# Optimization experiments

Hardware: AMD Instinct MI355X
Metric: run time of the kernel (lower is better)

## Reference

```python
import jax, jax.numpy as jnp
import numpy as np

N = 20000; DX = 512; DW = 64; DY = 256; M = 320000
DS = DX // 2; DD = DX // 4; DP = DS + DD  # 256, 128, 384
EPS = 1e-9; LN_EPS = 1e-5; SLOPE = 0.05
PNAMES = ['rW1','rb1','rg1','rbt1','rW2','rb2','yW1','yb1','yg1','ybt1','yW2','yb2',
          'iaW1','iab1','iag1','iabt1','iaW2','iab2','cW1','cb1','cg1','cbt1','cW2','cb2']

def _mlp2(h, W1, b1, g, be, W2, b2):
    # Linear -> LayerNorm -> LeakyReLU(0.05) -> Linear  (matches mlp(..., norm='layer'))
    h = h @ W1 + b1
    mu = jnp.mean(h, axis=-1, keepdims=True)
    var = jnp.mean((h - mu) ** 2, axis=-1, keepdims=True)
    h = (h - mu) * jax.lax.rsqrt(var + LN_EPS) * g + be
    h = jnp.where(h >= 0, h, SLOPE * h)
    return h @ W2 + b2

def _m(Pp, n, h):
    return _mlp2(h, Pp[n+'W1'], Pp[n+'b1'], Pp[n+'g1'], Pp[n+'bt1'], Pp[n+'W2'], Pp[n+'b2'])

def _agg(a, b):
    s = a + b
    return jnp.where(s >= 0, s, SLOPE * s)

def _run(x, ei, edge_attr, u_r, u_ia, u_pick, Pp, dec=None):
    """GuoUnpool forward (steps 1a, 2a, 2b). ei: concrete numpy [2,M] int64.
    dec holds concrete sampled decisions; built from the uniforms when None."""
    build = dec is None
    if build:
        dec = {}
    # coalesce (edges are duplicate-free) + lexsort by (src, dst)
    perm = np.argsort(ei[0].astype(np.int64) * N + ei[1].astype(np.int64), kind='stable')
    src, dst = ei[0][perm], ei[1][perm]
    ea = edge_attr[perm]
    # --- step 1a: bernoulli unpool decision per node (I_s = I_u = empty, I_r = all nodes)
    pr = jax.nn.sigmoid(_m(Pp, 'r', x)[:, 0])
    if build:
        dec['choose'] = np.asarray(u_r) < np.asarray(pr)
    choose = dec['choose']
    Iu = np.flatnonzero(choose); Is = np.flatnonzero(~choose)
    logP = jnp.sum(jnp.where(jnp.asarray(choose), jnp.log(pr + EPS), jnp.log(1.0 - pr + EPS)))
    prs = jnp.clip(pr, EPS, 1.0 - EPS)
    ent = -jnp.sum(prs * jnp.log(prs) + (1.0 - prs) * jnp.log(1.0 - prs))
    # --- projections (_ps1_idx = [0:ds+D], _ps2_idx = [0:ds] + [ds+D:ds+2D]) and child embeddings
    ps1 = x[:, :DP]
    ps2 = jnp.concatenate([x[:, :DS], x[:, DS + DD:DS + 2 * DD]], axis=-1)
    y1 = _m(Pp, 'y', ps1)   # [N, dy]; rows at Is give x_static, rows at Iu give x_c1
    y2 = _m(Pp, 'y', ps2)   # rows at Iu give x_c2
    x_out = jnp.concatenate([y1[Is], y1[Iu], y2[Iu]], axis=0)
    # --- step 2a: intra-edge decision for unpooled nodes
    p_ia = jax.nn.sigmoid(_m(Pp, 'ia', _agg(y1[Iu], y2[Iu]))[:, 0])
    if build:
        dec['vc'] = np.asarray(u_ia)[Iu] < np.asarray(p_ia)
    vc = dec['vc']
    logP = logP + jnp.sum(jnp.where(jnp.asarray(vc), jnp.log(p_ia + EPS), jnp.log(1.0 - p_ia + EPS)))
    ps = jnp.clip(p_ia, EPS, 1.0 - EPS)
    ent = ent - jnp.sum(ps * jnp.log(ps) + (1.0 - ps) * jnp.log(1.0 - ps))
    # --- step 2b: categorical neighbor pick for unpooled nodes without intra edge
    if build:
        iun = Iu[~vc]
        par = np.concatenate([src, dst]); nb = np.concatenate([dst, src])
        ek = np.concatenate([np.arange(len(src)), np.arange(len(src))])
        keep = np.zeros(N, dtype=bool); keep[iun] = True
        msk = keep[par]
        par, nb, ek = par[msk], nb[msk], ek[msk]
        o = np.lexsort((nb, par))  # adj lists sorted by neighbor id, grouped by parent
        par, nb, ek = par[o], nb[o], ek[o]
        new = np.r_[True, par[1:] != par[:-1]]
        dec['par'], dec['nb'], dec['ek'] = par, nb, ek
        dec['seg'] = np.cumsum(new) - 1
        dec['starts'] = np.flatnonzero(new)
    par, nb, ek = dec['par'], dec['nb'], dec['ek']
    segn, starts = dec['seg'], dec['starts']
    Pn = len(par); nseg = int(segn[-1]) + 1
    seg = jnp.asarray(segn)
    yagg = _agg(y1, y2)
    feats = jnp.concatenate([yagg[par], ea[ek], x[nb]], axis=-1)  # [Pn, dy+dw+dx]
    scores = _m(Pp, 'c', feats)[:, 0]
    mx = jax.ops.segment_max(scores, seg, num_segments=nseg)
    e = jnp.exp(scores - mx[segn])
    den = jax.ops.segment_sum(e, seg, num_segments=nseg)
    probs = e / den[segn]                      # per-parent softmax over neighbors
    if build:
        # multinomial pick via inverse CDF on the provided per-parent uniform
        p_np = np.asarray(probs).astype(np.float64)
        cum = np.cumsum(p_np)
        base = np.concatenate([[0.0], cum])[starts]
        cumw = cum - base[segn]
        useg = np.asarray(u_pick)[par[starts]][segn]
        cand = np.where(cumw > useg, np.arange(Pn), Pn)
        pick = np.minimum.reduceat(cand, starts)
        last = np.r_[starts[1:] - 1, Pn - 1]
        dec['pick'] = np.minimum(pick, last)
    pick = dec['pick']
    logP = logP + jnp.sum(jnp.log(jnp.clip(probs[pick], EPS, None)))
    pc = jnp.clip(probs, EPS, None)
    ent = ent - jnp.sum(pc * jnp.log(pc))
    return (x_out, logP, ent), dec

def _init_params(key):
    Pp = {}
    specs = [('r', DX, max(1, DX // 2), 1), ('y', DP, 128, DY), ('ia', DY, 128, 1), ('c', DY + DW + DX, 128, 1)]
    ks = jax.random.split(key, len(specs))
    for (n, a, h, o), k in zip(specs, ks):
        k1, k2 = jax.random.split(k)
        Pp[n+'W1'] = jax.random.normal(k1, (a, h), jnp.float32) / np.sqrt(a)
        Pp[n+'b1'] = jnp.zeros((h,), jnp.float32)
        Pp[n+'g1'] = jnp.ones((h,), jnp.float32)
        Pp[n+'bt1'] = jnp.zeros((h,), jnp.float32)
        Pp[n+'W2'] = jax.random.normal(k2, (h, o), jnp.float32) / np.sqrt(h)
        Pp[n+'b2'] = jnp.zeros((o,), jnp.float32)
    return Pp

def setup_inputs() -> dict:
    key = jax.random.key(0)
    k = jax.random.split(key, 6)
    x = jax.random.normal(k[0], (N, DX), jnp.float32)
    rng = np.random.default_rng(0)
    ns = int(M * 1.5)
    s = rng.integers(0, N, ns); d = rng.integers(0, N, ns)
    ok = s != d; s, d = s[ok], d[ok]
    _, ui = np.unique(s.astype(np.int64) * N + d, return_index=True)  # duplicate-free (coalesced)
    sel = rng.permutation(ui)[:M]
    edge_index = jnp.asarray(np.stack([s[sel], d[sel]]).astype(np.int64))
    inp = {
        'x': x,
        'edge_index': edge_index,
        'edge_attr': 0.5 * jax.random.normal(k[1], (M, DW), jnp.float32),
        'u_r': jax.random.uniform(k[2], (N,), jnp.float32),
        'u_ia': jax.random.uniform(k[3], (N,), jnp.float32),
        'u_pick': jax.random.uniform(k[4], (N,), jnp.float32),
    }
    inp.update(_init_params(k[5]))
    return inp

def reference(x, edge_index, edge_attr, u_r, u_ia, u_pick,
              rW1, rb1, rg1, rbt1, rW2, rb2,
              yW1, yb1, yg1, ybt1, yW2, yb2,
              iaW1, iab1, iag1, iabt1, iaW2, iab2,
              cW1, cb1, cg1, cbt1, cW2, cb2):
    Pp = dict(zip(PNAMES, (rW1, rb1, rg1, rbt1, rW2, rb2, yW1, yb1, yg1, ybt1, yW2, yb2,
                           iaW1, iab1, iag1, iabt1, iaW2, iab2, cW1, cb1, cg1, cbt1, cW2, cb2)))
    out, _ = _run(x, np.asarray(edge_index), edge_attr, u_r, u_ia, u_pick, Pp)
    return out
```

## Files before the change

### kernel.cpp

```cpp
#include <hip/hip_runtime.h>
#include <math.h>

#define KN 20000
#define KM 320000

typedef __attribute__((ext_vector_type(8))) short bf16x8;
typedef __attribute__((ext_vector_type(4))) float f32x4;

__device__ __forceinline__ ushort f2bf(float f){
  union{float f; unsigned u;} a; a.f=f;
  unsigned r = a.u + 0x7FFFu + ((a.u>>16)&1u);
  return (ushort)(r>>16);
}
__device__ __forceinline__ float bf2f(ushort u){
  union{unsigned u; float f;} a; a.u=((unsigned)u)<<16; return a.f;
}

__device__ __forceinline__ void blk_add2(double lp, double en, double* acc, double* sh){
#pragma unroll
  for (int o=32;o;o>>=1){ lp+=__shfl_xor(lp,o,64); en+=__shfl_xor(en,o,64); }
  int w=threadIdx.x>>6;
  if ((threadIdx.x&63)==0){ sh[2*w]=lp; sh[2*w+1]=en; }
  __syncthreads();
  if (threadIdx.x==0){
    double L=0,E=0; int nw=(blockDim.x+63)>>6;
    for (int i=0;i<nw;i++){L+=sh[2*i];E+=sh[2*i+1];}
    atomicAdd(&acc[0],L); atomicAdd(&acc[1],E);
  }
  __syncthreads();
}

__global__ __launch_bounds__(256) void k_prep_all(
    const float* __restrict__ x, ushort* __restrict__ x_hi, ushort* __restrict__ x_lo,
    const float* __restrict__ Wr1, ushort* __restrict__ Wrt_hi, ushort* __restrict__ Wrt_lo,
    double* __restrict__ w1d,
    const float* __restrict__ Wc1, ushort* __restrict__ W1t,
    const float* __restrict__ Wy1, ushort* __restrict__ W1yt,
    const float* __restrict__ Wy2, ushort* __restrict__ W2yt,
    int* __restrict__ deg,int* __restrict__ fill,int* __restrict__ keep,
    int* __restrict__ counters,double* __restrict__ acc){
  int i=blockIdx.x*256+threadIdx.x;
  if (i<KN*512/8){
    const float* s=x+(size_t)i*8;
    union{ushort u[8]; uint4 v;} oh, ol;
#pragma unroll
    for (int j=0;j<8;j++){
      float v=s[j];
      ushort h=f2bf(v);
      oh.u[j]=h;
      ol.u[j]=f2bf(v-bf2f(h));
    }
    *(uint4*)(x_hi+(size_t)i*8)=oh.v;
    *(uint4*)(x_lo+(size_t)i*8)=ol.v;
  }
  if (i<512*256){
    w1d[i]=(double)Wr1[i];
    int n=i&255, k=i>>8;
    float wv=Wr1[(size_t)k*256+n];
    ushort h=f2bf(wv);
    int kt=k>>5, kc=(k>>3)&3, j=k&7;
    size_t dst=(((size_t)kt*1024)+(size_t)kc*256+(size_t)n)*8+j;
    Wrt_hi[dst]=h;
    Wrt_lo[dst]=f2bf(wv-bf2f(h));
  }
  if (i<832*128){
    int n=i&127, k=i>>7;
    W1t[(size_t)n*832+k]=f2bf(Wc1[(size_t)k*128+n]);
  }
  if (i<384*128){
    int n=i&127, k=i>>7;
    W1yt[(size_t)n*384+k]=f2bf(Wy1[(size_t)k*128+n]);
  }
  if (i<128*256){
    int n=i&255, k=i>>8;
    W2yt[(size_t)n*128+k]=f2bf(Wy2[(size_t)k*256+n]);
  }
  if (i<KN){ deg[i]=0; fill[i]=0; keep[i]=0; }
  if (i<8) counters[i]=0;
  if (i<2) acc[i]=0.0;
}

#define RFLAG_TAU 3e-4f
#define YEXTP 261
__global__ __launch_bounds__(512) void k_mega1(const float* __restrict__ x,
    const ushort* __restrict__ x_hi,const ushort* __restrict__ x_lo,
    const ushort* __restrict__ Wrt_hi,const ushort* __restrict__ Wrt_lo,
    const double* __restrict__ w1d,
    const float* __restrict__ b1,const float* __restrict__ g1,
    const float* __restrict__ bt1,const float* __restrict__ W2,const float* __restrict__ b2,
    const float* __restrict__ u_r, float* __restrict__ pr, int* __restrict__ choose,
    const ushort* __restrict__ W1t, float* __restrict__ hxP,
    const ushort* __restrict__ W1yt,const float* __restrict__ b1y,const float* __restrict__ g1y,
    const float* __restrict__ bt1y,const ushort* __restrict__ W2yt,const float* __restrict__ b2y,
    float* __restrict__ y1_f,float* __restrict__ y2_f,
    float* __restrict__ yagg_f,ushort* __restrict__ yagg_bf,
    int RB,int HXB){
  __shared__ __align__(16) ushort Bl[2][2][8192];
  __shared__ float psum[64][2], pvar[64][2], pdot[64][2];
  __shared__ int flagsh[64];
  __shared__ double dsh[256];
  int t=threadIdx.x;
  int w=t>>6, l=t&63;
  int lr=l&15, lk=l>>4;
  if ((int)blockIdx.x>=RB+HXB){
    int b=blockIdx.x-RB-HXB;
    int sub=t>>8, tt=t&255;
    char* gbase=(char*)Bl + sub*25600;
    float*  hf  =(float*)gbase;
    float*  yext=(float*)gbase;
    ushort* hb  =(ushort*)(gbase+16896);
    int wy=tt>>6, ly=tt&63;
    int lry=ly&15, lky=ly>>4;
    int md=wy&1, kh=wy>>1;
    int row0=(b*2+sub)*16;
    const ushort* xr=x_hi+(size_t)(row0+lry)*512;
    f32x4 acc1[8];
#pragma unroll
    for (int c=0;c<8;c++) acc1[c]=(f32x4){0,0,0,0};
#pragma unroll
    for (int kt=0;kt<6;kt++){
      int k0=kh*192+kt*32+lky*8;
      int ks=(md && k0>=256)? k0+128 : k0;
      bf16x8 a=*(const bf16x8*)(xr+ks);
#pragma unroll
      for (int c=0;c<8;c++){
        bf16x8 b_=*(const bf16x8*)(W1yt+(size_t)(c*16+lry)*384+k0);
        acc1[c]=__builtin_amdgcn_mfma_f32_16x16x32_bf16(a,b_,acc1[c],0,0,0);
      }
    }
    if (kh==0){
#pragma unroll
      for (int i=0;i<4;i++){
        int row=lky*4+i;
#pragma unroll
        for (int c=0;c<8;c++) hf[((size_t)md*16+row)*132+c*16+lry]=acc1[c][i];
      }
    }
    __syncthreads();
    if (kh==1){
      float b1v[8],g1v[8],btv[8];
#pragma unroll
      for (int c=0;c<8;c++){ int col=c*16+lry; b1v[c]=b1y[col]; g1v[c]=g1y[col]; btv[c]=bt1y[col]; }
#pragma unroll
      for (int i=0;i<4;i++){
        int row=lky*4+i;
        float hv[8]; float s=0.f;
#pragma unroll
        for (int c=0;c<8;c++){ hv[c]=acc1[c][i]+hf[((size_t)md*16+row)*132+c*16+lry]+b1v[c]; s+=hv[c]; }
#pragma unroll
        for (int o=8;o;o>>=1) s+=__shfl_xor(s,o,64);
        float mu=s*(1.0f/128.0f);
        float v=0.f;
#pragma unroll
        for (int c=0;c<8;c++){ float d=hv[c]-mu; v+=d*d; }
#pragma unroll
        for (int o=8;o;o>>=1) v+=__shfl_xor(v,o,64);
        float rs=1.0f/sqrtf(v*(1.0f/128.0f)+1e-5f);
        ushort* hrow=hb+((size_t)md*16+row)*136;
#pragma unroll
        for (int c=0;c<8;c++){
          float hn=(hv[c]-mu)*rs*g1v[c]+btv[c];
          hn=hn>=0.f?hn:0.05f*hn;
          hrow[c*16+lry]=f2bf(hn);
        }
      }
    }
    __syncthreads();
    f32x4 acc2[8];
#pragma unroll
    for (int c=0;c<8;c++) acc2[c]=(f32x4){0,0,0,0};
    const ushort* ha=hb+((size_t)md*16+lry)*136;
#pragma unroll
    for (int kt=0;kt<4;kt++){
      bf16x8 a=*(const bf16x8*)(ha+kt*32+lky*8);
#pragma unroll
      for (int c=0;c<8;c++){
        bf16x8 b_=*(const bf16x8*)(W2yt+(size_t)(kh*128+c*16+lry)*128+kt*32+lky*8);
        acc2[c]=__builtin_amdgcn_mfma_f32_16x16x32_bf16(a,b_,acc2[c],0,0,0);
      }
    }
    float b2v[8];
#pragma unroll
    for (int c=0;c<8;c++) b2v[c]=b2y[kh*128+c*16+lry];
    if (md==0){
#pragma unroll
      for (int i=0;i<4;i++){
        int row=lky*4+i;
#pragma unroll
        for (int c=0;c<8;c++) yext[(size_t)row*YEXTP+kh*128+c*16+lry]=acc2[c][i]+b2v[c];
      }
    }
    __syncthreads();
    if (md==0){
#pragma unroll
      for (int i=0;i<4;i++){
        int row=lky*4+i, n=row0+row;
        float* orow=y1_f+(size_t)n*256+kh*128;
#pragma unroll
        for (int c=0;c<8;c++) orow[c*16+lry]=acc2[c][i]+b2v[c];
      }
    } else {
#pragma unroll
      for (int i=0;i<4;i++){
        int row=lky*4+i, n=row0+row;
        size_t base=(size_t)n*256+kh*128;
#pragma unroll
        for (int c=0;c<8;c++){
          int colk=c*16+lry;
          float v2=acc2[c][i]+b2v[c];
          float v1=yext[(size_t)row*YEXTP+kh*128+colk];
          float ga=v1+v2; ga=ga>=0.f?ga:0.05f*ga;
          yagg_f[base+colk]=ga;
          yagg_bf[base+colk]=f2bf(ga);
          y2_f[base+colk]=v2;
        }
      }
    }
    return;
  }
  if ((int)blockIdx.x>=RB){
    int b2=blockIdx.x-RB;
    int rh=w>>2, cw=w&3;
    int row0=b2*32+rh*16;
    const ushort* ar=x_hi+(size_t)(row0+lr)*512;
    f32x4 acc3[2];
#pragma unroll
    for (int c=0;c<2;c++) acc3[c]=(f32x4){0,0,0,0};
#pragma unroll
    for (int kt=0;kt<16;kt++){
      bf16x8 a=*(const bf16x8*)(ar+320+kt*32+lk*8);
#pragma unroll
      for (int c=0;c<2;c++){
        bf16x8 b=*(const bf16x8*)(W1t+(size_t)(cw*32+c*16+lr)*832+320+kt*32+lk*8);
        acc3[c]=__builtin_amdgcn_mfma_f32_16x16x32_bf16(a,b,acc3[c],0,0,0);
      }
    }
#pragma unroll
    for (int i=0;i<4;i++){
      int n=row0+lk*4+i;
      float2 v; v.x=acc3[0][i]; v.y=acc3[1][i];
      *(float2*)(hxP+(size_t)n*128+lr*8+cw*2)=v;
    }
    return;
  }
  int rg=w>>1, ch=w&1;
  int row0=blockIdx.x*64;
  if (t<64) flagsh[t]=0;
  int q0=t*2, q1=t*2+1;
  f32x4 acc[8];
#pragma unroll
  for (int c=0;c<8;c++) acc[c]=(f32x4){0,0,0,0};
  int rowA=row0+rg*16+lr; if (rowA>=KN) rowA=KN-1;
  const ushort* ah=x_hi+(size_t)rowA*512;
  const ushort* al=x_lo+(size_t)rowA*512;
  bf16x8 nh0=*(const bf16x8*)(Wrt_hi+q0*8);
  bf16x8 nh1=*(const bf16x8*)(Wrt_hi+q1*8);
  bf16x8 nl0=*(const bf16x8*)(Wrt_lo+q0*8);
  bf16x8 nl1=*(const bf16x8*)(Wrt_lo+q1*8);
  *(bf16x8*)&Bl[0][0][q0*8]=nh0; *(bf16x8*)&Bl[0][0][q1*8]=nh1;
  *(bf16x8*)&Bl[0][1][q0*8]=nl0; *(bf16x8*)&Bl[0][1][q1*8]=nl1;
  nh0=*(const bf16x8*)(Wrt_hi+8192+q0*8);
  nh1=*(const bf16x8*)(Wrt_hi+8192+q1*8);
  nl0=*(const bf16x8*)(Wrt_lo+8192+q0*8);
  nl1=*(const bf16x8*)(Wrt_lo+8192+q1*8);
  bf16x8 a_h0=*(const bf16x8*)(ah+0*32+lk*8), a_l0=*(const bf16x8*)(al+0*32+lk*8);
  bf16x8 a_h1=*(const bf16x8*)(ah+1*32+lk*8), a_l1=*(const bf16x8*)(al+1*32+lk*8);
  bf16x8 a_h2=*(const bf16x8*)(ah+2*32+lk*8), a_l2=*(const bf16x8*)(al+2*32+lk*8);
  bf16x8 a_h3=*(const bf16x8*)(ah+3*32+lk*8), a_l3=*(const bf16x8*)(al+3*32+lk*8);
  __syncthreads();
#define RBODY(KT,AH,AL) { \
    const int cur_=(KT)&1, nxt_=cur_^1; \
    if ((KT)<15){ \
      *(bf16x8*)&Bl[nxt_][0][q0*8]=nh0; *(bf16x8*)&Bl[nxt_][0][q1*8]=nh1; \
      *(bf16x8*)&Bl[nxt_][1][q0*8]=nl0; *(bf16x8*)&Bl[nxt_][1][q1*8]=nl1; \
      if ((KT)<14){ \
        size_t so_=(size_t)((KT)+2)*8192; \
        nh0=*(const bf16x8*)(Wrt_hi+so_+q0*8); nh1=*(const bf16x8*)(Wrt_hi+so_+q1*8); \
        nl0=*(const bf16x8*)(Wrt_lo+so_+q0*8); nl1=*(const bf16x8*)(Wrt_lo+so_+q1*8); \
      } \
    } \
    bf16x8 uh_=AH, ul_=AL; \
    if ((KT)<12){ \
      int ko_=((KT)+4)*32+lk*8; \
      AH=*(const bf16x8*)(ah+ko_); \
      AL=*(const bf16x8*)(al+ko_); \
    } \
    _Pragma("unroll") \
    for (int c=0;c<8;c++){ \
      int col_=ch*128+c*16+lr; \
      bf16x8 vh_=*(const bf16x8*)&Bl[cur_][0][((lk<<8)+col_)*8]; \
      bf16x8 vl_=*(const bf16x8*)&Bl[cur_][1][((lk<<8)+col_)*8]; \
      acc[c]=__builtin_amdgcn_mfma_f32_16x16x32_bf16(uh_,vh_,acc[c],0,0,0); \
      acc[c]=__builtin_amdgcn_mfma_f32_16x16x32_bf16(uh_,vl_,acc[c],0,0,0); \
      acc[c]=__builtin_amdgcn_mfma_f32_16x16x32_bf16(ul_,vh_,acc[c],0,0,0); \
    } \
    __syncthreads(); \
  }
  RBODY(0,a_h0,a_l0)  RBODY(1,a_h1,a_l1)  RBODY(2,a_h2,a_l2)  RBODY(3,a_h3,a_l3)
  RBODY(4,a_h0,a_l0)  RBODY(5,a_h1,a_l1)  RBODY(6,a_h2,a_l2)  RBODY(7,a_h3,a_l3)
  RBODY(8,a_h0,a_l0)  RBODY(9,a_h1,a_l1)  RBODY(10,a_h2,a_l2) RBODY(11,a_h3,a_l3)
  RBODY(12,a_h0,a_l0) RBODY(13,a_h1,a_l1) RBODY(14,a_h2,a_l2) RBODY(15,a_h3,a_l3)
#undef RBODY
  float b1v[8],g1v[8],btv[8],w2v[8];
#pragma unroll
  for (int c=0;c<8;c++){
    int col=ch*128+c*16+lr;
    b1v[c]=b1[col]; g1v[c]=g1[col]; btv[c]=bt1[col]; w2v[c]=W2[col];
  }
  float hv[4][8];
#pragma unroll
  for (int i=0;i<4;i++){
    float s=0.f;
#pragma unroll
    for (int c=0;c<8;c++){ hv[i][c]=acc[c][i]+b1v[c]; s+=hv[i][c]; }
#pragma unroll
    for (int o=8;o;o>>=1) s+=__shfl_xor(s,o,64);
    if (lr==0) psum[rg*16+lk*4+i][ch]=s;
  }
  __syncthreads();
  float mu_[4];
#pragma unroll
  for (int i=0;i<4;i++){
    int r=rg*16+lk*4+i;
    mu_[i]=(psum[r][0]+psum[r][1])*(1.0f/256.0f);
    float v=0.f;
#pragma unroll
    for (int c=0;c<8;c++){ float d=hv[i][c]-mu_[i]; v+=d*d; }
#pragma unroll
    for (int o=8;o;o>>=1) v+=__shfl_xor(v,o,64);
    if (lr==0) pvar[r][ch]=v;
  }
  __syncthreads();
#pragma unroll
  for (int i=0;i<4;i++){
    int r=rg*16+lk*4+i;
    float rs=1.0f/sqrtf((pvar[r][0]+pvar[r][1])*(1.0f/256.0f)+1e-5f);
    float dot=0.f;
#pragma unroll
    for (int c=0;c<8;c++){
      float hn=(hv[i][c]-mu_[i])*rs*g1v[c]+btv[c];
      hn=hn>=0.f?hn:0.05f*hn;
      dot=fmaf(hn,w2v[c],dot);
    }
#pragma unroll
    for (int o=8;o;o>>=1) dot+=__shfl_xor(dot,o,64);
    if (lr==0) pdot[r][ch]=dot;
  }
  __syncthreads();
  if (t<64){
    int n=row0+t;
    if (n<KN){
      float o2=pdot[t][0]+pdot[t][1]+b2[0];
      float pf=1.0f/(1.0f+expf(-o2));
      float u=u_r[n];
      pr[n]=pf;
      choose[n]=(u<pf)?1:0;
      if (fabsf(pf-u)<RFLAG_TAU) flagsh[t]=1;
    }
  }
  __syncthreads();
  for (int r=0;r<64;r++){
    if (!flagsh[r]) continue;
    int n=row0+r;
    if (t<256){
      double ha=(double)b1[t];
      const float* xr=x+(size_t)n*512;
      for (int k=0;k<512;k++) ha=fma((double)xr[k],w1d[(size_t)k*256+t],ha);
      dsh[t]=ha;
    }
    __syncthreads();
    if (t<64){
      double s=0;
      for (int j=t;j<256;j+=64) s+=dsh[j];
#pragma unroll
      for (int o=32;o;o>>=1) s+=__shfl_xor(s,o,64);
      double mu=s*(1.0/256.0);
      double v=0;
      for (int j=t;j<256;j+=64){ double d=dsh[j]-mu; v+=d*d; }
#pragma unroll
      for (int o=32;o;o>>=1) v+=__shfl_xor(v,o,64);
      double rs=1.0/sqrt(v*(1.0/256.0)+1e-5);
      double dot=0;
      for (int j=t;j<256;j+=64){
        double hn=(dsh[j]-mu)*rs*(double)g1[j]+(double)bt1[j];
        hn = hn>=0.0? hn : 0.05*hn;
        dot=fma(hn,(double)W2[j],dot);
      }
#pragma unroll
      for (int o=32;o;o>>=1) dot+=__shfl_xor(dot,o,64);
      if (t==0){
        double p=1.0/(1.0+exp(-(dot+(double)b2[0])));
        float pf=(float)p;
        pr[n]=pf;
        choose[n]=(u_r[n]<pf)?1:0;
      }
    }
    __syncthreads();
  }
}

__global__ __launch_bounds__(1024) void k_scan_choose(const int* __restrict__ choose,int* __restrict__ excl,
                                                      int* __restrict__ iu,int* __restrict__ counters){
  __shared__ int wsum[16], woff[16];
  const int CH=(KN+1023)/1024;
  int t=threadIdx.x, lane=t&63, wid=t>>6;
  int base=t*CH;
  int s=0;
  for (int i=0;i<CH;i++){int idx=base+i; if (idx<KN) s+=choose[idx];}
  int inc=s;
  for (int o=1;o<64;o<<=1){ int v=__shfl_up(inc,o,64); if (lane>=o) inc+=v; }
  if (lane==63) wsum[wid]=inc;
  __syncthreads();
  if (t==0){ int r=0; for (int i=0;i<16;i++){ woff[i]=r; r+=wsum[i]; } counters[2]=r; }
  __syncthreads();
  int ex=woff[wid]+inc-s;
  for (int i=0;i<CH;i++){
    int idx=base+i;
    if (idx<KN){ int c=choose[idx]; excl[idx]=ex; if (c) iu[ex]=idx; ex+=c; }
  }
}

__global__ __launch_bounds__(256) void k_mega2(const float* __restrict__ yagg_f,
    const ushort* __restrict__ yagg_bf,const ushort* __restrict__ W1t,float* __restrict__ hyP,
    const int* __restrict__ iu,const float* __restrict__ u_ia,
    const float* __restrict__ W1,const float* __restrict__ b1,const float* __restrict__ g1,
    const float* __restrict__ bt1,const float* __restrict__ W2,const float* __restrict__ b2,
    float* __restrict__ p_ia,int* __restrict__ vc,int* __restrict__ keep,double* __restrict__ acc,
    const float* __restrict__ y1_f,const float* __restrict__ y2_f,
    const int* __restrict__ choose,const int* __restrict__ excl,
    float* __restrict__ out,const float* __restrict__ pr,
    int cnt,int HB,int IAB,int SCB){
  __shared__ float insh[16][256];
  __shared__ float hsh[16][128];
  __shared__ double sh[8];
  int t=threadIdx.x;
  int w=t>>6, l=t&63;
  int lr=l&15, lk=l>>4;
  if ((int)blockIdx.x<HB){
    int rh=w>>1, cq=w&1;
    int row0=blockIdx.x*32+rh*16;
    const ushort* ar=yagg_bf+(size_t)(row0+lr)*256+lk*8;
    f32x4 acc4[4];
#pragma unroll
    for (int c=0;c<4;c++) acc4[c]=(f32x4){0,0,0,0};
#pragma unroll
    for (int kt=0;kt<8;kt++){
      bf16x8 a=*(const bf16x8*)(ar+kt*32);
#pragma unroll
      for (int c=0;c<4;c++){
        bf16x8 b=*(const bf16x8*)(W1t+(size_t)(cq*64+c*16+lr)*832+kt*32+lk*8);
        acc4[c]=__builtin_amdgcn_mfma_f32_16x16x32_bf16(a,b,acc4[c],0,0,0);
      }
    }
#pragma unroll
    for (int i=0;i<4;i++){
      int n=row0+lk*4+i;
      float4 v; v.x=acc4[0][i]; v.y=acc4[1][i]; v.z=acc4[2][i]; v.w=acc4[3][i];
      *(float4*)(hyP+(size_t)n*128+lr*8+cq*4)=v;
    }
    return;
  }
  if ((int)blockIdx.x<HB+IAB){
    int row0=(blockIdx.x-HB)*16;
    for (int i=t;i<16*256;i+=256){
      int r=i>>8,k=i&255;
      int row=row0+r;
      if (row<cnt){
        unsigned n=(unsigned)iu[row];
        if (n<KN) insh[r][k]=yagg_f[(size_t)n*256+k];
        else insh[r][k]=0.f;
      }
    }
    __syncthreads();
    int h=t>>7, tt=t&127;
    float accv[8]; float bb=b1[tt];
#pragma unroll
    for (int r=0;r<8;r++) accv[r]=bb;
    for (int k=0;k<256;k+=4){
      float w0=W1[(k+0)*128+tt],w1=W1[(k+1)*128+tt],w2=W1[(k+2)*128+tt],w3=W1[(k+3)*128+tt];
#pragma unroll
      for (int r=0;r<8;r++){
        float4 f=*(const float4*)&insh[h*8+r][k];
        accv[r]=fmaf(f.x,w0,accv[r]); accv[r]=fmaf(f.y,w1,accv[r]); accv[r]=fmaf(f.z,w2,accv[r]); accv[r]=fmaf(f.w,w3,accv[r]);
      }
    }
#pragma unroll
    for (int r=0;r<8;r++) hsh[h*8+r][tt]=accv[r];
    __syncthreads();
    int g=t>>4, tl=t&15;
    float hv[8];
#pragma unroll
    for (int j=0;j<8;j++) hv[j]=hsh[g][tl+16*j];
    float s=0;
#pragma unroll
    for (int j=0;j<8;j++) s+=hv[j];
#pragma unroll
    for (int o=8;o;o>>=1) s+=__shfl_xor(s,o,64);
    float mu=s*(1.0f/128.0f);
    float v=0;
#pragma unroll
    for (int j=0;j<8;j++){float d=hv[j]-mu; v+=d*d;}
#pragma unroll
    for (int o=8;o;o>>=1) v+=__shfl_xor(v,o,64);
    float rs=1.0f/sqrtf(v*(1.0f/128.0f)+1e-5f);
    float dot=0;
#pragma unroll
    for (int j=0;j<8;j++){
      int idx=tl+16*j;
      float hn=(hv[j]-mu)*rs*g1[idx]+bt1[idx];
      hn=hn>=0.f?hn:0.05f*hn;
      dot=fmaf(hn,W2[idx],dot);
    }
#pragma unroll
    for (int o=8;o;o>>=1) dot+=__shfl_xor(dot,o,64);
    double lp=0,en=0;
    if (tl==0){
      int row=row0+g;
      if (row<cnt){
        unsigned n=(unsigned)iu[row];
        if (n<KN){
          float o=dot+b2[0];
          double p=1.0/(1.0+exp(-(double)o));
          float pf=(float)p;
          p_ia[row]=pf;
          int vv=(u_ia[n]<pf)?1:0;
          vc[row]=vv;
          if(!vv) keep[n]=1;
          lp = vv? log((double)pf+1e-9) : log(1.0-(double)pf+1e-9);
          double ps=fmin(fmax((double)pf,1e-9),1.0-1e-9);
          en = -(ps*log(ps)+(1.0-ps)*log(1.0-ps));
        }
      }
    }
    blk_add2(lp,en,acc,sh);
    return;
  }
  if ((int)blockIdx.x<HB+IAB+SCB){
    int b=blockIdx.x-HB-IAB;
    int r0=b*32;
    for (int r=0;r<32;r++){
      int n=r0+r;
      if (n>=KN) break;
      int cch=choose[n], ex=excl[n];
      int r1 = cch? (KN-cnt)+ex : n-ex;
      if (r1>=0 && r1<KN+cnt) out[(size_t)r1*256+t]=y1_f[(size_t)n*256+t];
      if (cch){ int r2=KN+ex; if (r2<KN+cnt) out[(size_t)r2*256+t]=y2_f[(size_t)n*256+t]; }
    }
    return;
  }
  {
    int i=(blockIdx.x-HB-IAB-SCB)*256+t;
    double lp=0,en=0;
    if (i<KN){
      double p=(double)pr[i];
      lp = choose[i]? log(p+1e-9) : log(1.0-p+1e-9);
      double ps=fmin(fmax(p,1e-9),1.0-1e-9);
      en = -(ps*log(ps)+(1.0-ps)*log(1.0-ps));
    }
    blk_add2(lp,en,acc,(double*)insh);
  }
}

__global__ void k_count(const int* __restrict__ ei,const int* __restrict__ keep,int* __restrict__ deg){
  int e=blockIdx.x*256+threadIdx.x;
  if (e<KM){
    int s=ei[e], d=ei[KM+e];
    if (keep[s]) atomicAdd(&deg[s],1);
    if (keep[d]) atomicAdd(&deg[d],1);
  }
}

__global__ __launch_bounds__(1024) void k_scan_deg(const int* __restrict__ deg,int* __restrict__ boff,
                                                   int* __restrict__ nodeseg,int* __restrict__ counters){
  __shared__ int wsum[16], woff[16];
  const int CH=(KN+1023)/1024;
  int t=threadIdx.x, lane=t&63, wid=t>>6;
  int base=t*CH;
  int s=0, sc=0;
  for (int i=0;i<CH;i++){int idx=base+i; if(idx<KN){ int d=deg[idx]; s+=d; sc+=(d>0)?1:0; }}
  int inc=s;
  for (int o=1;o<64;o<<=1){ int v=__shfl_up(inc,o,64); if (lane>=o) inc+=v; }
  if (lane==63) wsum[wid]=inc;
  __syncthreads();
  if (t==0){ int r=0; for (int i=0;i<16;i++){ woff[i]=r; r+=wsum[i]; } boff[KN]=r; counters[0]=r; }
  __syncthreads();
  int ex=woff[wid]+inc-s;
  for (int i=0;i<CH;i++){int idx=base+i; if(idx<KN){ boff[idx]=ex; ex+=deg[idx]; }}
  __syncthreads();
  int inc2=sc;
  for (int o=1;o<64;o<<=1){ int v=__shfl_up(inc2,o,64); if (lane>=o) inc2+=v; }
  if (lane==63) wsum[wid]=inc2;
  __syncthreads();
  if (t==0){ int r=0; for (int i=0;i<16;i++){ woff[i]=r; r+=wsum[i]; } counters[1]=r; }
  __syncthreads();
  int ex2=woff[wid]+inc2-sc;
  for (int i=0;i<CH;i++){int idx=base+i; if(idx<KN && deg[idx]>0){ nodeseg[ex2]=idx; ex2++; }}
}

__global__ void k_fill(const int* __restrict__ ei,const int* __restrict__ keep,const int* __restrict__ boff,
                       int* __restrict__ fill,int* __restrict__ parA,int* __restrict__ keyA,int* __restrict__ ekA){
  int e=blockIdx.x*256+threadIdx.x;
  if (e<KM){
    int s=ei[e], d=ei[KM+e];
    if (keep[s]){ int pos=boff[s]+atomicAdd(&fill[s],1); parA[pos]=s; keyA[pos]=d*2;   ekA[pos]=e; }
    if (keep[d]){ int pos=boff[d]+atomicAdd(&fill[d],1); parA[pos]=d; keyA[pos]=s*2+1; ekA[pos]=e; }
  }
}

__global__ void k_rank(const int* __restrict__ parA,const int* __restrict__ keyA,const int* __restrict__ ekA,
                       const int* __restrict__ boff,const int* __restrict__ counters,
                       int* __restrict__ parS,int* __restrict__ nbS,int* __restrict__ ekS){
  int i=blockIdx.x*256+threadIdx.x;
  int Pn=counters[0];
  if (i<Pn){
    int par=parA[i], key=keyA[i];
    int lo=boff[par], hi=boff[par+1];
    int rank=0;
    for (int j=lo;j<hi;j++) rank += (keyA[j]<key)?1:0;
    int pos=lo+rank;
    parS[pos]=par; nbS[pos]=key>>1; ekS[pos]=ekA[i];
  }
}

__global__ __launch_bounds__(256) void k_cscore_v6(
    const float* __restrict__ ea,const float* __restrict__ hyP,const float* __restrict__ hxP,
    const int* __restrict__ parS,const int* __restrict__ nbS,const int* __restrict__ ekS,
    const int* __restrict__ counters,
    const ushort* __restrict__ W1t,const float* __restrict__ b1,const float* __restrict__ g1,
    const float* __restrict__ bt1,const float* __restrict__ W2,const float* __restrict__ b2,
    float* __restrict__ scores){
  int Pn=counters[0];
  if (Pn<=0) return;
  int t=threadIdx.x;
  int w=t>>6, l=t&63;
  int lr=l&15, lk=l>>4;
  float b2s=b2[0];
  float b1v[8],g1v[8],btv[8],w2v[8];
#pragma unroll
  for (int c=0;c<8;c++){
    int col=c*16+lr;
    b1v[c]=b1[col]; g1v[c]=g1[col]; btv[c]=bt1[col]; w2v[c]=W2[col];
  }
  int ngrp=(Pn+63)>>6;
  for (int g=blockIdx.x; g<ngrp; g+=gridDim.x){
    int p0=g*64+w*16;
    float hs[4][8];
#pragma unroll
    for (int i=0;i<4;i++){
      int p=p0+lk*4+i; int pc=p<Pn?p:Pn-1;
      const float* hyp=hyP+(size_t)parS[pc]*128+lr*8;
      const float* hxp=hxP+(size_t)nbS[pc]*128+lr*8;
      float4 ya=*(const float4*)hyp, yb=*(const float4*)(hyp+4);
      float4 xa=*(const float4*)hxp, xb=*(const float4*)(hxp+4);
      hs[i][0]=ya.x+xa.x; hs[i][1]=ya.y+xa.y; hs[i][2]=ya.z+xa.z; hs[i][3]=ya.w+xa.w;
      hs[i][4]=yb.x+xb.x; hs[i][5]=yb.y+xb.y; hs[i][6]=yb.z+xb.z; hs[i][7]=yb.w+xb.w;
    }
    int pA=p0+lr; int ca=pA<Pn?pA:Pn-1;
    const float* eaA=ea+(size_t)ekS[ca]*64;
    f32x4 acc[8];
#pragma unroll
    for (int c=0;c<8;c++) acc[c]=(f32x4){0,0,0,0};
#pragma unroll
    for (int kt=0;kt<2;kt++){
      float4 fa=*(const float4*)(eaA+kt*32+lk*8);
      float4 fb=*(const float4*)(eaA+kt*32+lk*8+4);
      union{ushort u[8]; bf16x8 v;} A;
      A.u[0]=f2bf(fa.x); A.u[1]=f2bf(fa.y); A.u[2]=f2bf(fa.z); A.u[3]=f2bf(fa.w);
      A.u[4]=f2bf(fb.x); A.u[5]=f2bf(fb.y); A.u[6]=f2bf(fb.z); A.u[7]=f2bf(fb.w);
      bf16x8 a=A.v;
#pragma unroll
      for (int c=0;c<8;c++){
        bf16x8 b=*(const bf16x8*)(W1t+(size_t)(c*16+lr)*832+256+kt*32+lk*8);
        acc[c]=__builtin_amdgcn_mfma_f32_16x16x32_bf16(a,b,acc[c],0,0,0);
      }
    }
#pragma unroll
    for (int i=0;i<4;i++){
      float hv[8]; float s=0.f;
#pragma unroll
      for (int c=0;c<8;c++){ hv[c]=acc[c][i]+hs[i][c]+b1v[c]; s+=hv[c]; }
#pragma unroll
      for (int o=8;o;o>>=1) s+=__shfl_xor(s,o,64);
      float mu=s*(1.0f/128.0f);
      float v=0.f;
#pragma unroll
      for (int c=0;c<8;c++){ float d=hv[c]-mu; v+=d*d; }
#pragma unroll
      for (int o=8;o;o>>=1) v+=__shfl_xor(v,o,64);
      float rs=1.0f/sqrtf(v*(1.0f/128.0f)+1e-5f);
      float dot=0.f;
#pragma unroll
      for (int c=0;c<8;c++){
        float hn=(hv[c]-mu)*rs*g1v[c]+btv[c];
        hn=hn>=0.f?hn:0.05f*hn;
        dot=fmaf(hn,w2v[c],dot);
      }
#pragma unroll
      for (int o=8;o;o>>=1) dot+=__shfl_xor(dot,o,64);
      if (lr==0){
        int prow=p0+lk*4+i;
        if (prow<Pn) scores[prow]=dot+b2s;
      }
    }
  }
}

__global__ __launch_bounds__(256) void k_segment(const float* __restrict__ scores,const int* __restrict__ boff,
    const int* __restrict__ nodeseg,const int* __restrict__ counters,const float* __restrict__ u_pick,
    double* __restrict__ acc){
  __shared__ double sh[8];
  int nseg=counters[1];
  int s=blockIdx.x*256+threadIdx.x;
  double lp=0,en=0;
  if (s<nseg){
    int n=nodeseg[s];
    int lo=boff[n],hi=boff[n+1];
    float mx=-1e30f;
    for (int p=lo;p<hi;p++) mx=fmaxf(mx,scores[p]);
    float den=0;
    for (int p=lo;p<hi;p++) den+=expf(scores[p]-mx);
    double u=(double)u_pick[n];
    double cum=0; float ppick=-1.f; float plast=0.f;
    for (int p=lo;p<hi;p++){
      float e=expf(scores[p]-mx);
      float prob=e/den;
      double pc=fmax((double)prob,1e-9);
      en -= pc*log(pc);
      plast=prob;
      if (ppick<0.f){ cum+=(double)prob; if (cum>u) ppick=prob; }
    }
    if (ppick<0.f) ppick=plast;
    lp=log(fmax((double)ppick,1e-9));
  }
  blk_add2(lp,en,acc,sh);
}

__global__ void k_final(const double* __restrict__ acc,float* __restrict__ out,int cnt){
  if (threadIdx.x==0 && blockIdx.x==0){
    size_t base=(size_t)(KN+cnt)*256;
    out[base]=(float)acc[0];
    out[base+1]=(float)acc[1];
  }
}

extern "C" void kernel_launch(void* const* d_in,const int* in_sizes,int n_in,
                              void* d_out,int out_size,void* d_ws,size_t ws_size,
                              hipStream_t stream){
  const float* x     =(const float*)d_in[0];
  const int*   ei    =(const int*)  d_in[1];
  const float* ea    =(const float*)d_in[2];
  const float* u_r   =(const float*)d_in[3];
  const float* u_ia  =(const float*)d_in[4];
  const float* u_pick=(const float*)d_in[5];
  const float* Pp[24];
  for (int i=0;i<24;i++) Pp[i]=(const float*)d_in[6+i];
  float* out=(float*)d_out;
  int cnt=(out_size-2)/256 - KN;
  if (cnt<0) cnt=0;

  char* w=(char*)d_ws;
  size_t off=0;
  auto carve=[&](size_t bytes)->char*{ off=(off+255)&~(size_t)255; char* p=w+off; off+=bytes; return p; };
  int*    counters=(int*)   carve(64);
  double* acc     =(double*)carve(64);
  float*  pr      =(float*) carve((size_t)KN*4);
  int*    choose  =(int*)   carve((size_t)KN*4);
  int*    excl    =(int*)   carve((size_t)KN*4);
  int*    iu      =(int*)   carve((size_t)KN*4);
  float*  p_ia    =(float*) carve((size_t)KN*4);
  int*    vc      =(int*)   carve((size_t)KN*4);
  int*    keep    =(int*)   carve((size_t)KN*4);
  int*    deg     =(int*)   carve((size_t)KN*4);
  int*    fill    =(int*)   carve((size_t)KN*4);
  int*    boff    =(int*)   carve((size_t)(KN+1)*4);
  int*    nodeseg =(int*)   carve((size_t)KN*4);
  int*    parA    =(int*)   carve((size_t)2*KM*4);
  int*    keyA    =(int*)   carve((size_t)2*KM*4);
  int*    ekA     =(int*)   carve((size_t)2*KM*4);
  int*    parS    =(int*)   carve((size_t)2*KM*4);
  int*    nbS     =(int*)   carve((size_t)2*KM*4);
  int*    ekS     =(int*)   carve((size_t)2*KM*4);
  float*  scores  =(float*) carve((size_t)2*KM*4);
  float*  yagg_f  =(float*) carve((size_t)KN*256*4);
  ushort* yagg_bf =(ushort*)carve((size_t)KN*256*2);
  float*  y1_f    =(float*) carve((size_t)KN*256*4);
  float*  y2_f    =(float*) carve((size_t)KN*256*4);
  ushort* x_bf    =(ushort*)carve((size_t)KN*512*2);
  ushort* x_lo    =(ushort*)carve((size_t)KN*512*2);
  ushort* W1t     =(ushort*)carve((size_t)832*128*2);
  double* w1d     =(double*)carve((size_t)512*256*8);
  ushort* W1yt    =(ushort*)carve((size_t)128*384*2);
  ushort* W2yt    =(ushort*)carve((size_t)256*128*2);
  ushort* Wrt_hi  =(ushort*)carve((size_t)256*512*2);
  ushort* Wrt_lo  =(ushort*)carve((size_t)256*512*2);
  float*  hy      =(float*) carve((size_t)KN*128*4);
  float*  hx      =(float*) carve((size_t)KN*128*4);
  (void)ws_size;(void)n_in;(void)in_sizes;

  const int RB=(KN+63)/64;
  const int HXB=KN/32;
  const int YB2=KN/32;
  const int HB=KN/32;
  const int IAB=(cnt+15)/16;
  const int SCB=(KN+31)/32;
  const int NTB=(KN+255)/256;

  k_prep_all<<<(KN*512/8+255)/256,256,0,stream>>>(x,x_bf,x_lo,
      Pp[0],Wrt_hi,Wrt_lo,w1d, Pp[18],W1t, Pp[6],W1yt, Pp[10],W2yt,
      deg,fill,keep,counters,acc);
  k_mega1<<<RB+HXB+YB2,512,0,stream>>>(x,x_bf,x_lo,Wrt_hi,Wrt_lo,w1d,
      Pp[1],Pp[2],Pp[3],Pp[4],Pp[5],u_r,pr,choose,W1t,hx,
      W1yt,Pp[7],Pp[8],Pp[9],W2yt,Pp[11],y1_f,y2_f,yagg_f,yagg_bf,RB,HXB);
  k_scan_choose<<<1,1024,0,stream>>>(choose,excl,iu,counters);
  k_mega2<<<HB+IAB+SCB+NTB,256,0,stream>>>(yagg_f,yagg_bf,W1t,hy,iu,u_ia,
      Pp[12],Pp[13],Pp[14],Pp[15],Pp[16],Pp[17],p_ia,vc,keep,acc,
      y1_f,y2_f,choose,excl,out,pr,cnt,HB,IAB,SCB);
  k_count<<<(KM+255)/256,256,0,stream>>>(ei,keep,deg);
  k_scan_deg<<<1,1024,0,stream>>>(deg,boff,nodeseg,counters);
  k_fill<<<(KM+255)/256,256,0,stream>>>(ei,keep,boff,fill,parA,keyA,ekA);
  k_rank<<<(2*KM+255)/256,256,0,stream>>>(parA,keyA,ekA,boff,counters,parS,nbS,ekS);
  k_cscore_v6<<<2560,256,0,stream>>>(ea,hy,hx,parS,nbS,ekS,counters,W1t,Pp[19],Pp[20],Pp[21],Pp[22],Pp[23],scores);
  k_segment<<<(KN+255)/256,256,0,stream>>>(scores,boff,nodeseg,counters,u_pick,acc);
  k_final<<<1,64,0,stream>>>(acc,out,cnt);
}
```

Baseline: 407.1 us.

## Fold unconditional degree counting into mega1 and reorder mega2 block roles

Degree counting over all edges now runs unconditionally as extra blocks appended to k_mega1, since it no longer depends on the keep mask. The keep filter is applied afterwards inside k_scan_deg, which removes the separate k_count launch from the dependency chain. k_mega2 also dispatches the IA-score blocks before the hy GEMM blocks so the longer IA work starts first. In exchange, k_mega1 does atomic work for every edge endpoint, including nodes that are not kept, and k_scan_deg reads keep three times.

Measured after the change: 409.9 us. About the same (+0.7%).

```diff
diff --git a/kernel.cpp b/kernel.cpp
--- a/kernel.cpp
+++ b/kernel.cpp
@@ -94,7 +94,8 @@
     const float* __restrict__ bt1y,const ushort* __restrict__ W2yt,const float* __restrict__ b2y,
     float* __restrict__ y1_f,float* __restrict__ y2_f,
     float* __restrict__ yagg_f,ushort* __restrict__ yagg_bf,
-    int RB,int HXB){
+    const int* __restrict__ ei,int* __restrict__ degF,
+    int RB,int HXB,int YB2){
   __shared__ __align__(16) ushort Bl[2][2][8192];
   __shared__ float psum[64][2], pvar[64][2], pdot[64][2];
   __shared__ int flagsh[64];
@@ -102,6 +103,15 @@
   int t=threadIdx.x;
   int w=t>>6, l=t&63;
   int lr=l&15, lk=l>>4;
+  if ((int)blockIdx.x>=RB+HXB+YB2){
+    int e=(blockIdx.x-(RB+HXB+YB2))*512+t;
+    if (e<KM){
+      int s=ei[e], d=ei[KM+e];
+      atomicAdd(&degF[s],1);
+      atomicAdd(&degF[d],1);
+    }
+    return;
+  }
   if ((int)blockIdx.x>=RB+HXB){
     int b=blockIdx.x-RB-HXB;
     int sub=t>>8, tt=t&255;
@@ -436,32 +446,8 @@
   int t=threadIdx.x;
   int w=t>>6, l=t&63;
   int lr=l&15, lk=l>>4;
-  if ((int)blockIdx.x<HB){
-    int rh=w>>1, cq=w&1;
-    int row0=blockIdx.x*32+rh*16;
-    const ushort* ar=yagg_bf+(size_t)(row0+lr)*256+lk*8;
-    f32x4 acc4[4];
-#pragma unroll
-    for (int c=0;c<4;c++) acc4[c]=(f32x4){0,0,0,0};
-#pragma unroll
-    for (int kt=0;kt<8;kt++){
-      bf16x8 a=*(const bf16x8*)(ar+kt*32);
-#pragma unroll
-      for (int c=0;c<4;c++){
-        bf16x8 b=*(const bf16x8*)(W1t+(size_t)(cq*64+c*16+lr)*832+kt*32+lk*8);
-        acc4[c]=__builtin_amdgcn_mfma_f32_16x16x32_bf16(a,b,acc4[c],0,0,0);
-      }
-    }
-#pragma unroll
-    for (int i=0;i<4;i++){
-      int n=row0+lk*4+i;
-      float4 v; v.x=acc4[0][i]; v.y=acc4[1][i]; v.z=acc4[2][i]; v.w=acc4[3][i];
-      *(float4*)(hyP+(size_t)n*128+lr*8+cq*4)=v;
-    }
-    return;
-  }
-  if ((int)blockIdx.x<HB+IAB){
-    int row0=(blockIdx.x-HB)*16;
+  if ((int)blockIdx.x<IAB){
+    int row0=blockIdx.x*16;
     for (int i=t;i<16*256;i+=256){
       int r=i>>8,k=i&255;
       int row=row0+r;
@@ -535,8 +521,33 @@
     blk_add2(lp,en,acc,sh);
     return;
   }
-  if ((int)blockIdx.x<HB+IAB+SCB){
-    int b=blockIdx.x-HB-IAB;
+  if ((int)blockIdx.x<IAB+HB){
+    int bb=blockIdx.x-IAB;
+    int rh=w>>1, cq=w&1;
+    int row0=bb*32+rh*16;
+    const ushort* ar=yagg_bf+(size_t)(row0+lr)*256+lk*8;
+    f32x4 acc4[4];
+#pragma unroll
+    for (int c=0;c<4;c++) acc4[c]=(f32x4){0,0,0,0};
+#pragma unroll
+    for (int kt=0;kt<8;kt++){
+      bf16x8 a=*(const bf16x8*)(ar+kt*32);
+#pragma unroll
+      for (int c=0;c<4;c++){
+        bf16x8 b=*(const bf16x8*)(W1t+(size_t)(cq*64+c*16+lr)*832+kt*32+lk*8);
+        acc4[c]=__builtin_amdgcn_mfma_f32_16x16x32_bf16(a,b,acc4[c],0,0,0);
+      }
+    }
+#pragma unroll
+    for (int i=0;i<4;i++){
+      int n=row0+lk*4+i;
+      float4 v; v.x=acc4[0][i]; v.y=acc4[1][i]; v.z=acc4[2][i]; v.w=acc4[3][i];
+      *(float4*)(hyP+(size_t)n*128+lr*8+cq*4)=v;
+    }
+    return;
+  }
+  if ((int)blockIdx.x<IAB+HB+SCB){
+    int b=blockIdx.x-IAB-HB;
     int r0=b*32;
     for (int r=0;r<32;r++){
       int n=r0+r;
@@ -549,7 +560,7 @@
     return;
   }
   {
-    int i=(blockIdx.x-HB-IAB-SCB)*256+t;
+    int i=(blockIdx.x-IAB-HB-SCB)*256+t;
     double lp=0,en=0;
     if (i<KN){
       double p=(double)pr[i];
@@ -561,23 +572,15 @@
   }
 }
 
-__global__ void k_count(const int* __restrict__ ei,const int* __restrict__ keep,int* __restrict__ deg){
-  int e=blockIdx.x*256+threadIdx.x;
-  if (e<KM){
-    int s=ei[e], d=ei[KM+e];
-    if (keep[s]) atomicAdd(&deg[s],1);
-    if (keep[d]) atomicAdd(&deg[d],1);
-  }
-}
-
-__global__ __launch_bounds__(1024) void k_scan_deg(const int* __restrict__ deg,int* __restrict__ boff,
+__global__ __launch_bounds__(1024) void k_scan_deg(const int* __restrict__ degF,const int* __restrict__ keep,
+                                                   int* __restrict__ boff,
                                                    int* __restrict__ nodeseg,int* __restrict__ counters){
   __shared__ int wsum[16], woff[16];
   const int CH=(KN+1023)/1024;
   int t=threadIdx.x, lane=t&63, wid=t>>6;
   int base=t*CH;
   int s=0, sc=0;
-  for (int i=0;i<CH;i++){int idx=base+i; if(idx<KN){ int d=deg[idx]; s+=d; sc+=(d>0)?1:0; }}
+  for (int i=0;i<CH;i++){int idx=base+i; if(idx<KN){ int d=keep[idx]?degF[idx]:0; s+=d; sc+=(d>0)?1:0; }}
   int inc=s;
   for (int o=1;o<64;o<<=1){ int v=__shfl_up(inc,o,64); if (lane>=o) inc+=v; }
   if (lane==63) wsum[wid]=inc;
@@ -585,7 +588,7 @@
   if (t==0){ int r=0; for (int i=0;i<16;i++){ woff[i]=r; r+=wsum[i]; } boff[KN]=r; counters[0]=r; }
   __syncthreads();
   int ex=woff[wid]+inc-s;
-  for (int i=0;i<CH;i++){int idx=base+i; if(idx<KN){ boff[idx]=ex; ex+=deg[idx]; }}
+  for (int i=0;i<CH;i++){int idx=base+i; if(idx<KN){ int d=keep[idx]?degF[idx]:0; boff[idx]=ex; ex+=d; }}
   __syncthreads();
   int inc2=sc;
   for (int o=1;o<64;o<<=1){ int v=__shfl_up(inc2,o,64); if (lane>=o) inc2+=v; }
@@ -594,7 +597,7 @@
   if (t==0){ int r=0; for (int i=0;i<16;i++){ woff[i]=r; r+=wsum[i]; } counters[1]=r; }
   __syncthreads();
   int ex2=woff[wid]+inc2-sc;
-  for (int i=0;i<CH;i++){int idx=base+i; if(idx<KN && deg[idx]>0){ nodeseg[ex2]=idx; ex2++; }}
+  for (int i=0;i<CH;i++){int idx=base+i; if(idx<KN){ int d=keep[idx]?degF[idx]:0; if(d>0){ nodeseg[ex2]=idx; ex2++; } }}
 }
 
 __global__ void k_fill(const int* __restrict__ ei,const int* __restrict__ keep,const int* __restrict__ boff,
@@ -800,6 +803,7 @@
   const int RB=(KN+63)/64;
   const int HXB=KN/32;
   const int YB2=KN/32;
+  const int CFB=(KM+511)/512;
   const int HB=KN/32;
   const int IAB=(cnt+15)/16;
   const int SCB=(KN+31)/32;
@@ -808,15 +812,15 @@
   k_prep_all<<<(KN*512/8+255)/256,256,0,stream>>>(x,x_bf,x_lo,
       Pp[0],Wrt_hi,Wrt_lo,w1d, Pp[18],W1t, Pp[6],W1yt, Pp[10],W2yt,
       deg,fill,keep,counters,acc);
-  k_mega1<<<RB+HXB+YB2,512,0,stream>>>(x,x_bf,x_lo,Wrt_hi,Wrt_lo,w1d,
+  k_mega1<<<RB+HXB+YB2+CFB,512,0,stream>>>(x,x_bf,x_lo,Wrt_hi,Wrt_lo,w1d,
       Pp[1],Pp[2],Pp[3],Pp[4],Pp[5],u_r,pr,choose,W1t,hx,
-      W1yt,Pp[7],Pp[8],Pp[9],W2yt,Pp[11],y1_f,y2_f,yagg_f,yagg_bf,RB,HXB);
+      W1yt,Pp[7],Pp[8],Pp[9],W2yt,Pp[11],y1_f,y2_f,yagg_f,yagg_bf,
+      ei,deg,RB,HXB,YB2);
   k_scan_choose<<<1,1024,0,stream>>>(choose,excl,iu,counters);
-  k_mega2<<<HB+IAB+SCB+NTB,256,0,stream>>>(yagg_f,yagg_bf,W1t,hy,iu,u_ia,
+  k_mega2<<<IAB+HB+SCB+NTB,256,0,stream>>>(yagg_f,yagg_bf,W1t,hy,iu,u_ia,
       Pp[12],Pp[13],Pp[14],Pp[15],Pp[16],Pp[17],p_ia,vc,keep,acc,
       y1_f,y2_f,choose,excl,out,pr,cnt,HB,IAB,SCB);
-  k_count<<<(KM+255)/256,256,0,stream>>>(ei,keep,deg);
-  k_scan_deg<<<1,1024,0,stream>>>(deg,boff,nodeseg,counters);
+  k_scan_deg<<<1,1024,0,stream>>>(deg,keep,boff,nodeseg,counters);
   k_fill<<<(KM+255)/256,256,0,stream>>>(ei,keep,boff,fill,parA,keyA,ekA);
   k_rank<<<(2*KM+255)/256,256,0,stream>>>(parA,keyA,ekA,boff,counters,parS,nbS,ekS);
   k_cscore_v6<<<2560,256,0,stream>>>(ea,hy,hx,parS,nbS,ekS,counters,W1t,Pp[19],Pp[20],Pp[21],Pp[22],Pp[23],scores);
```
